# Kernel tuning notes

Measured on AMD Instinct MI355X. Metric: run time of the kernel, lower is better.

The kernel has to match this reference:

```python
import jax, jax.numpy as jnp
import numpy as np

EPS = 1e-6
NEG_SLOPE = 0.2
LN_EPS = 1e-6


def _evn_nonlinearity(x, wa, ba, wb, bb):
    # x: (..., F, D); norm over the vector axis F (axis=-2)
    norm = jnp.linalg.norm(x, axis=-2, keepdims=True)  # (..., 1, D)
    zero_norm = norm <= EPS
    norm = norm + EPS
    h = jax.nn.leaky_relu(norm @ wa + ba, NEG_SLOPE)   # (..., 1, D//2)
    g = h @ wb + bb                                    # (..., 1, D)
    # skip_connection == 0: rescale direction by learned norm gate
    return jnp.where(zero_norm, x, x / norm * g)


def _layernorm(x, scale, bias):
    mean = jnp.mean(x, axis=-1, keepdims=True)
    var = jnp.var(x, axis=-1, keepdims=True)
    return (x - mean) * jax.lax.rsqrt(var + LN_EPS) * scale + bias


def setup_inputs() -> dict:
    key = jax.random.key(0)
    ks = jax.random.split(key, 12)
    B, N, F, D = 8, 2048, 3, 256
    QK, V, H, Q = 512, 512, 8, 64
    dh, dv = QK // H, V // H
    s = lambda *sh: 1.0 / np.sqrt(sh[0])
    return {
        "x": jax.random.normal(ks[0], (B, N, F, D), jnp.float32),
        "lq": jax.random.normal(ks[1], (Q, QK), jnp.float32) * s(QK),
        "w_kv": jax.random.normal(ks[2], (D, QK), jnp.float32) * s(D),
        "w_evn1a": jax.random.normal(ks[3], (QK, QK // 2), jnp.float32) * s(QK),
        "b_evn1a": jnp.zeros((QK // 2,), jnp.float32),
        "w_evn1b": jax.random.normal(ks[4], (QK // 2, QK), jnp.float32) * s(QK // 2),
        "b_evn1b": jnp.zeros((QK,), jnp.float32),
        "wq": jax.random.normal(ks[5], (QK, H, dh), jnp.float32) * s(QK),
        "wk": jax.random.normal(ks[6], (QK, H, dh), jnp.float32) * s(QK),
        "wv": jax.random.normal(ks[7], (QK, H, dv), jnp.float32) * s(QK),
        "ln_q_scale": jnp.ones((dh,), jnp.float32),
        "ln_q_bias": jnp.zeros((dh,), jnp.float32),
        "ln_k_scale": jnp.ones((dh,), jnp.float32),
        "ln_k_bias": jnp.zeros((dh,), jnp.float32),
        "w_out": jax.random.normal(ks[8], (V, V), jnp.float32) * s(V),
        "w_evn2a": jax.random.normal(ks[9], (V, V // 2), jnp.float32) * s(V),
        "b_evn2a": jnp.zeros((V // 2,), jnp.float32),
        "w_evn2b": jax.random.normal(ks[10], (V // 2, V), jnp.float32) * s(V // 2),
        "b_evn2b": jnp.zeros((V,), jnp.float32),
    }


def reference(x, lq, w_kv, w_evn1a, b_evn1a, w_evn1b, b_evn1b, wq, wk, wv,
              ln_q_scale, ln_q_bias, ln_k_scale, ln_k_bias,
              w_out, w_evn2a, b_evn2a, w_evn2b, b_evn2b):
    B, N, F, _ = x.shape
    H = wq.shape[1]
    # EVLinearLeakyReLU: Dense (no bias) + EVN nonlinearity
    kv = _evn_nonlinearity(x @ w_kv, w_evn1a, b_evn1a, w_evn1b, b_evn1b)  # (B,N,F,QK)
    # invariant features: contract vector axis with its channel-mean
    kv_inv = jnp.einsum('bnfd,bnf->bnd', kv, jnp.mean(kv, axis=-1))       # (B,N,QK)
    q = jnp.einsum('qd,dhe->hqe', lq, wq)          # (H,Q,dh)
    k = jnp.einsum('bnd,dhe->hbne', kv_inv, wk)    # (H,B,N,dh)
    v = jnp.einsum('bnfd,dhe->hbnfe', kv, wv)      # (H,B,N,F,dv)
    # normalize_qk
    q = _layernorm(q, ln_q_scale, ln_q_bias)
    k = _layernorm(k, ln_k_scale, ln_k_bias)
    scale = np.sqrt(k.shape[-1]).astype(np.float32)
    attn = jnp.einsum('hqi,hbki->hbqk', q, k)      # (H,B,Q,N)
    attn = jax.nn.softmax(attn / scale, axis=-1)
    resi = jnp.einsum('hbqk,hbkfd->hbqfd', attn, v)  # (H,B,Q,F,dv)
    # 'h b q f d -> b q f (h d)'
    resi = jnp.moveaxis(resi, 0, -2)
    resi = resi.reshape(*resi.shape[:-2], -1)        # (B,Q,F,V)
    resi = _evn_nonlinearity(resi @ w_out, w_evn2a, b_evn2a, w_evn2b, b_evn2b)
    return resi
```

## Files before the change

### kernel.cpp

```cpp
#include <hip/hip_runtime.h>
#include <hip/hip_bf16.h>

typedef _Float16 f16;
typedef __attribute__((ext_vector_type(8))) _Float16 f16x8;
typedef __attribute__((ext_vector_type(4))) _Float16 f16x4;
typedef __attribute__((ext_vector_type(2))) _Float16 f16x2;
typedef __attribute__((ext_vector_type(4))) float floatx4;

constexpr int B  = 8;
constexpr int N  = 2048;
constexpr int Fv = 3;
constexpr int Dd = 256;
constexpr int QK = 512;
constexpr int Vd = 512;
constexpr int Hh = 8;
constexpr int Qq = 64;
constexpr int DH = 64;
constexpr int NT = B * N;
constexpr float EPS = 1e-6f;
constexpr float NEG = 0.2f;
constexpr float LNE = 1e-6f;

#define DEV static __device__ __forceinline__
DEV void split(float v, f16& h, f16& l) { h = (f16)v; l = (f16)(v - (float)h); }

template<int ASRC, int EPI>
__global__ __launch_bounds__(256) void k_gemm3(
    const float* __restrict__ A32,
    const f16* __restrict__ Ah, const f16* __restrict__ Al,
    const f16* __restrict__ Bh, const f16* __restrict__ Bl,
    int Ndim, int Kdim, void* __restrict__ C1, void* __restrict__ C2,
    const float* __restrict__ e0, const float* __restrict__ e1)
{
    __shared__ __align__(16) f16 Ash[128][72];
    __shared__ __align__(16) f16 Asl[128][72];
    __shared__ __align__(16) f16 Bsh[64][72];
    __shared__ __align__(16) f16 Bsl[64][72];

    const int t = threadIdx.x;
    long row0; int col0, boff;
    if (EPI == 5) { row0 = (long)blockIdx.y * 1536 + (long)blockIdx.x * 128; col0 = 0; boff = blockIdx.y * 64; }
    else          { row0 = (long)blockIdx.x * 128; col0 = blockIdx.y * 64; boff = 0; }

    floatx4 acc0[4], acc1[4];
    #pragma unroll
    for (int nt = 0; nt < 4; ++nt)
        #pragma unroll
        for (int j = 0; j < 4; ++j) { acc0[nt][j] = 0.f; acc1[nt][j] = 0.f; }

    const int L = t & 63, w = t >> 6;
    const int kq = (L >> 4) << 3;

    for (int k0 = 0; k0 < Kdim; k0 += 64) {
        if constexpr (ASRC == 1) {
            #pragma unroll
            for (int j = 0; j < 8; ++j) {
                const int i = t + j * 256;
                const int r = i >> 4, c4 = (i & 15) << 2;
                const floatx4 v = *(const floatx4*)&A32[(row0 + r) * Kdim + k0 + c4];
                f16x4 h4, l4;
                #pragma unroll
                for (int m = 0; m < 4; ++m) { h4[m] = (f16)v[m]; l4[m] = (f16)(v[m] - (float)h4[m]); }
                *(f16x4*)&Ash[r][c4] = h4;
                *(f16x4*)&Asl[r][c4] = l4;
            }
        } else {
            #pragma unroll
            for (int j = 0; j < 4; ++j) {
                const int i = t + j * 256;
                const int r = i >> 3, c8 = (i & 7) << 3;
                *(f16x8*)&Ash[r][c8] = *(const f16x8*)&Ah[(row0 + r) * (long)Kdim + k0 + c8];
                *(f16x8*)&Asl[r][c8] = *(const f16x8*)&Al[(row0 + r) * (long)Kdim + k0 + c8];
            }
        }
        #pragma unroll
        for (int j = 0; j < 2; ++j) {
            const int i = t + j * 256;
            const int r = i >> 3, c8 = (i & 7) << 3;
            *(f16x8*)&Bsh[r][c8] = *(const f16x8*)&Bh[(long)(boff + col0 + r) * Kdim + k0 + c8];
            *(f16x8*)&Bsl[r][c8] = *(const f16x8*)&Bl[(long)(boff + col0 + r) * Kdim + k0 + c8];
        }
        __syncthreads();
        #pragma unroll
        for (int kk = 0; kk < 64; kk += 32) {
            const f16x8 ah0 = *(const f16x8*)&Ash[w * 32 + (L & 15)][kk + kq];
            const f16x8 al0 = *(const f16x8*)&Asl[w * 32 + (L & 15)][kk + kq];
            const f16x8 ah1 = *(const f16x8*)&Ash[w * 32 + 16 + (L & 15)][kk + kq];
            const f16x8 al1 = *(const f16x8*)&Asl[w * 32 + 16 + (L & 15)][kk + kq];
            #pragma unroll
            for (int nt = 0; nt < 4; ++nt) {
                const f16x8 bh = *(const f16x8*)&Bsh[nt * 16 + (L & 15)][kk + kq];
                const f16x8 bl = *(const f16x8*)&Bsl[nt * 16 + (L & 15)][kk + kq];
                acc0[nt] = __builtin_amdgcn_mfma_f32_16x16x32_f16(ah0, bh, acc0[nt], 0, 0, 0);
                acc0[nt] = __builtin_amdgcn_mfma_f32_16x16x32_f16(ah0, bl, acc0[nt], 0, 0, 0);
                acc0[nt] = __builtin_amdgcn_mfma_f32_16x16x32_f16(al0, bh, acc0[nt], 0, 0, 0);
                acc1[nt] = __builtin_amdgcn_mfma_f32_16x16x32_f16(ah1, bh, acc1[nt], 0, 0, 0);
                acc1[nt] = __builtin_amdgcn_mfma_f32_16x16x32_f16(ah1, bl, acc1[nt], 0, 0, 0);
                acc1[nt] = __builtin_amdgcn_mfma_f32_16x16x32_f16(al1, bh, acc1[nt], 0, 0, 0);
            }
        }
        __syncthreads();
    }

    const int cb = L & 15;
    #pragma unroll
    for (int rt = 0; rt < 2; ++rt) {
        const floatx4* acc = rt ? acc1 : acc0;
        const int rb = w * 32 + rt * 16 + ((L >> 4) << 2);
        if constexpr (EPI == 0) {
            f16* Ch = (f16*)C1; f16* Cl = (f16*)C2;
            #pragma unroll
            for (int nt = 0; nt < 4; ++nt)
                #pragma unroll
                for (int r = 0; r < 4; ++r) {
                    f16 h, l; split(acc[nt][r], h, l);
                    const long o = (row0 + rb + r) * (long)Ndim + col0 + nt * 16 + cb;
                    Ch[o] = h; Cl[o] = l;
                }
        } else if constexpr (EPI == 1) {
            f16* Ch = (f16*)C1; f16* Cl = (f16*)C2;
            #pragma unroll
            for (int nt = 0; nt < 4; ++nt) {
                const int col = col0 + nt * 16 + cb;
                const float bias = e0[col];
                #pragma unroll
                for (int r = 0; r < 4; ++r) {
                    float v = acc[nt][r] + bias;
                    v = v > 0.f ? v : NEG * v;
                    f16 h, l; split(v, h, l);
                    const long o = (row0 + rb + r) * (long)Ndim + col;
                    Ch[o] = h; Cl[o] = l;
                }
            }
        } else if constexpr (EPI == 2) {
            float* C = (float*)C1;
            #pragma unroll
            for (int nt = 0; nt < 4; ++nt) {
                const int col = col0 + nt * 16 + cb;
                const float bias = e0[col];
                #pragma unroll
                for (int r = 0; r < 4; ++r)
                    C[(row0 + rb + r) * (long)Ndim + col] = acc[nt][r] + bias;
            }
        } else if constexpr (EPI == 3) {
            f16* Ch = (f16*)C1; f16* Cl = (f16*)C2;
            const int h = blockIdx.y;
            #pragma unroll
            for (int r = 0; r < 4; ++r) {
                float s = 0.f, q = 0.f;
                #pragma unroll
                for (int nt = 0; nt < 4; ++nt) { const float v = acc[nt][r]; s += v; q += v * v; }
                s += __shfl_xor(s, 1); q += __shfl_xor(q, 1);
                s += __shfl_xor(s, 2); q += __shfl_xor(q, 2);
                s += __shfl_xor(s, 4); q += __shfl_xor(q, 4);
                s += __shfl_xor(s, 8); q += __shfl_xor(q, 8);
                const float mean = s * (1.f / 64.f);
                const float var  = q * (1.f / 64.f) - mean * mean;
                const float rs   = rsqrtf(var + LNE);
                #pragma unroll
                for (int nt = 0; nt < 4; ++nt) {
                    const int col = nt * 16 + cb;
                    const float v = (acc[nt][r] - mean) * rs * e0[col] + e1[col];
                    f16 hh, ll; split(v, hh, ll);
                    const long o = ((long)h * NT + row0 + rb + r) * 64 + col;
                    Ch[o] = hh; Cl[o] = ll;
                }
            }
        } else {
            float* C = (float*)C1;
            #pragma unroll
            for (int nt = 0; nt < 4; ++nt)
                #pragma unroll
                for (int r = 0; r < 4; ++r) {
                    const long rr = row0 + rb + r - (long)blockIdx.y * 1536;
                    C[rr * 512 + boff + nt * 16 + cb] = acc[nt][r];
                }
        }
    }
}

__global__ __launch_bounds__(512, 4) void k_kv2(
    const float* __restrict__ x,
    const f16* __restrict__ Bh, const f16* __restrict__ Bl,
    f16* __restrict__ Ch, f16* __restrict__ Cl)
{
    __shared__ __align__(16) f16 Ash[2][128][32];
    __shared__ __align__(16) f16 Asl[2][128][32];
    __shared__ __align__(16) f16 Bsh[2][128][32];
    __shared__ __align__(16) f16 Bsl[2][128][32];

    const int t = threadIdx.x;
    const int bx = blockIdx.x;
    const long row0 = (long)(bx >> 2) * 128;
    const int col0 = (bx & 3) * 128;

    const int sr = t >> 2;
    const int sg = t & 3;
    const int spg = ((sg ^ ((sr >> 1) & 3)) << 3);
    const float* ap  = x  + (row0 + sr) * 256 + sg * 8;
    const f16*   bph = Bh + (long)(col0 + sr) * 256 + sg * 8;
    const f16*   bpl = Bl + (long)(col0 + sr) * 256 + sg * 8;

    floatx4 acc[2][4];
    #pragma unroll
    for (int rg = 0; rg < 2; ++rg)
        #pragma unroll
        for (int nt = 0; nt < 4; ++nt)
            #pragma unroll
            for (int j = 0; j < 4; ++j) acc[rg][nt][j] = 0.f;

    const int L = t & 63, w = t >> 6;
    const int wr = (w >> 1) << 5;
    const int wc = (w & 1) << 6;
    const int kqs = (((L >> 4) ^ ((L >> 1) & 3)) << 3);

    floatx4 pa0, pa1; f16x8 pbh, pbl;
    floatx4 qa0, qa1; f16x8 qbh, qbl;

    auto LOADA = [&](int k0) {
        pa0 = *(const floatx4*)&ap[k0];
        pa1 = *(const floatx4*)&ap[k0 + 4];
        pbh = *(const f16x8*)&bph[k0];
        pbl = *(const f16x8*)&bpl[k0];
    };
    auto LOADB = [&](int k0) {
        qa0 = *(const floatx4*)&ap[k0];
        qa1 = *(const floatx4*)&ap[k0 + 4];
        qbh = *(const f16x8*)&bph[k0];
        qbl = *(const f16x8*)&bpl[k0];
    };
    auto WRITEA = [&](int buf) {
        f16x8 h8, l8;
        #pragma unroll
        for (int m = 0; m < 4; ++m) {
            f16 hh, ll;
            split(pa0[m], hh, ll); h8[m] = hh;     l8[m] = ll;
            split(pa1[m], hh, ll); h8[m + 4] = hh; l8[m + 4] = ll;
        }
        *(f16x8*)&Ash[buf][sr][spg] = h8;
        *(f16x8*)&Asl[buf][sr][spg] = l8;
        *(f16x8*)&Bsh[buf][sr][spg] = pbh;
        *(f16x8*)&Bsl[buf][sr][spg] = pbl;
    };
    auto WRITEB = [&](int buf) {
        f16x8 h8, l8;
        #pragma unroll
        for (int m = 0; m < 4; ++m) {
            f16 hh, ll;
            split(qa0[m], hh, ll); h8[m] = hh;     l8[m] = ll;
            split(qa1[m], hh, ll); h8[m + 4] = hh; l8[m + 4] = ll;
        }
        *(f16x8*)&Ash[buf][sr][spg] = h8;
        *(f16x8*)&Asl[buf][sr][spg] = l8;
        *(f16x8*)&Bsh[buf][sr][spg] = qbh;
        *(f16x8*)&Bsl[buf][sr][spg] = qbl;
    };
    auto COMPUTE = [&](int buf) {
        const f16x8 ah0 = *(const f16x8*)&Ash[buf][wr + (L & 15)][kqs];
        const f16x8 al0 = *(const f16x8*)&Asl[buf][wr + (L & 15)][kqs];
        const f16x8 ah1 = *(const f16x8*)&Ash[buf][wr + 16 + (L & 15)][kqs];
        const f16x8 al1 = *(const f16x8*)&Asl[buf][wr + 16 + (L & 15)][kqs];
        #pragma unroll
        for (int nt = 0; nt < 4; ++nt) {
            const f16x8 bh = *(const f16x8*)&Bsh[buf][wc + nt * 16 + (L & 15)][kqs];
            const f16x8 bl = *(const f16x8*)&Bsl[buf][wc + nt * 16 + (L & 15)][kqs];
            acc[0][nt] = __builtin_amdgcn_mfma_f32_16x16x32_f16(ah0, bh, acc[0][nt], 0, 0, 0);
            acc[0][nt] = __builtin_amdgcn_mfma_f32_16x16x32_f16(ah0, bl, acc[0][nt], 0, 0, 0);
            acc[0][nt] = __builtin_amdgcn_mfma_f32_16x16x32_f16(al0, bh, acc[0][nt], 0, 0, 0);
            acc[1][nt] = __builtin_amdgcn_mfma_f32_16x16x32_f16(ah1, bh, acc[1][nt], 0, 0, 0);
            acc[1][nt] = __builtin_amdgcn_mfma_f32_16x16x32_f16(ah1, bl, acc[1][nt], 0, 0, 0);
            acc[1][nt] = __builtin_amdgcn_mfma_f32_16x16x32_f16(al1, bh, acc[1][nt], 0, 0, 0);
        }
    };

    LOADA(0);
    WRITEA(0);
    LOADA(32);
    __syncthreads();

    for (int tt = 0; tt < 8; tt += 2) {
        if (tt + 2 < 8) LOADB((tt + 2) * 32);
        COMPUTE(0);
        if (tt + 1 < 8) WRITEA(1);
        __syncthreads();
        if (tt + 3 < 8) LOADA((tt + 3) * 32);
        COMPUTE(1);
        if (tt + 2 < 8) WRITEB(0);
        __syncthreads();
    }

    const int cb = L & 15;
    #pragma unroll
    for (int rg = 0; rg < 2; ++rg) {
        const int rb = wr + rg * 16 + ((L >> 4) << 2);
        #pragma unroll
        for (int nt = 0; nt < 4; ++nt)
            #pragma unroll
            for (int r = 0; r < 4; ++r) {
                f16 h, l; split(acc[rg][nt][r], h, l);
                const long o = (row0 + rb + r) * 512 + col0 + wc + nt * 16 + cb;
                Ch[o] = h; Cl[o] = l;
            }
    }
}

__global__ __launch_bounds__(256) void k_attn_mfma(
    const f16* __restrict__ qh, const f16* __restrict__ ql,
    const f16* __restrict__ kh, const f16* __restrict__ kl,
    f16* __restrict__ ath, f16* __restrict__ atl, float* __restrict__ lsum_part)
{
    __shared__ __align__(16) f16 Qh[64][72], Ql[64][72];
    __shared__ __align__(16) f16 Kh[64][72], Kl[64][72];

    const int t = threadIdx.x;
    const int bx = blockIdx.x;
    const int hb = bx & 63;
    const int part = bx >> 6;
    const int h = hb >> 3;
    const int L = t & 63, w = t >> 6;
    const int kq = (L >> 4) << 3;

    #pragma unroll
    for (int j = 0; j < 2; ++j) {
        const int i = t + j * 256;
        const int r = i >> 3, c8 = (i & 7) << 3;
        *(f16x8*)&Qh[r][c8] = *(const f16x8*)&qh[((long)h * 64 + r) * 64 + c8];
        *(f16x8*)&Ql[r][c8] = *(const f16x8*)&ql[((long)h * 64 + r) * 64 + c8];
    }
    __syncthreads();

    f16x8 qah[2], qal[2];
    #pragma unroll
    for (int kc = 0; kc < 2; ++kc) {
        qah[kc] = *(const f16x8*)&Qh[w * 16 + (L & 15)][kc * 32 + kq];
        qal[kc] = *(const f16x8*)&Ql[w * 16 + (L & 15)][kc * 32 + kq];
    }

    float psum[4] = {0.f, 0.f, 0.f, 0.f};
    const int rowb = w * 16 + ((L >> 4) << 2);

    for (int nt0 = 0; nt0 < 4; ++nt0) {
        const int n0 = part * 256 + nt0 * 64;
        __syncthreads();
        #pragma unroll
        for (int j = 0; j < 2; ++j) {
            const int i = t + j * 256;
            const int r = i >> 3, c8 = (i & 7) << 3;
            *(f16x8*)&Kh[r][c8] = *(const f16x8*)&kh[((long)hb * N + n0 + r) * 64 + c8];
            *(f16x8*)&Kl[r][c8] = *(const f16x8*)&kl[((long)hb * N + n0 + r) * 64 + c8];
        }
        __syncthreads();

        floatx4 acc[4];
        #pragma unroll
        for (int nt = 0; nt < 4; ++nt)
            #pragma unroll
            for (int j = 0; j < 4; ++j) acc[nt][j] = 0.f;

        #pragma unroll
        for (int kc = 0; kc < 2; ++kc) {
            #pragma unroll
            for (int nt = 0; nt < 4; ++nt) {
                const f16x8 bh = *(const f16x8*)&Kh[nt * 16 + (L & 15)][kc * 32 + kq];
                const f16x8 bl = *(const f16x8*)&Kl[nt * 16 + (L & 15)][kc * 32 + kq];
                acc[nt] = __builtin_amdgcn_mfma_f32_16x16x32_f16(qah[kc], bh, acc[nt], 0, 0, 0);
                acc[nt] = __builtin_amdgcn_mfma_f32_16x16x32_f16(qah[kc], bl, acc[nt], 0, 0, 0);
                acc[nt] = __builtin_amdgcn_mfma_f32_16x16x32_f16(qal[kc], bh, acc[nt], 0, 0, 0);
            }
        }

        #pragma unroll
        for (int nt = 0; nt < 4; ++nt)
            #pragma unroll
            for (int r = 0; r < 4; ++r) {
                const float p = __expf(acc[nt][r] * 0.125f);
                psum[r] += p;
                f16 hh, ll; split(p, hh, ll);
                const long o = ((long)hb * 64 + rowb + r) * N + n0 + nt * 16 + (L & 15);
                ath[o] = hh; atl[o] = ll;
            }
    }

    #pragma unroll
    for (int r = 0; r < 4; ++r) {
        float s = psum[r];
        s += __shfl_xor(s, 1);
        s += __shfl_xor(s, 2);
        s += __shfl_xor(s, 4);
        s += __shfl_xor(s, 8);
        if ((L & 15) == 0) lsum_part[part * 4096 + hb * 64 + rowb + r] = s;
    }
}

__global__ void k_lsum_reduce(const float* __restrict__ part, float* __restrict__ lsum)
{
    const int i = blockIdx.x * 256 + threadIdx.x;
    float s = 0.f;
    #pragma unroll
    for (int p = 0; p < 8; ++p) s += part[p * 4096 + i];
    lsum[i] = s;
}

__global__ __launch_bounds__(512, 4) void k_gemm3T(
    const f16* __restrict__ Ah, const f16* __restrict__ Al,
    const f16* __restrict__ Bh, const f16* __restrict__ Bl,
    const float* __restrict__ lsum,
    f16* __restrict__ Uh, f16* __restrict__ Ul)
{
    __shared__ __align__(16) f16 Ash[2][128][32];
    __shared__ __align__(16) f16 Asl[2][128][32];
    __shared__ __align__(16) f16 Bsh[2][96][32];
    __shared__ __align__(16) f16 Bsl[2][96][32];

    const int t = threadIdx.x;
    const int by = blockIdx.x;
    const int b = by & 7;
    const int rest = by >> 3;
    const int ct = rest & 15;
    const int hp = rest >> 4;
    const int hb0 = b + 16 * hp;
    const int hb1 = hb0 + 8;

    const int ar = t >> 2;
    const int apg = (((t & 3) ^ ((t >> 3) & 3)) << 3);
    const f16* Arh = (ar < 64)
        ? Ah + ((long)hb0 * 64 + ar) * 2048
        : Ah + ((long)hb1 * 64 + (ar - 64)) * 2048;
    const f16* Arl = (ar < 64)
        ? Al + ((long)hb0 * 64 + ar) * 2048
        : Al + ((long)hb1 * 64 + (ar - 64)) * 2048;
    const int aseg = (t & 3) << 3;

    const f16* Bbh = Bh + (long)b * 2048 * 1536 + ct * 96;
    const f16* Bbl = Bl + (long)b * 2048 * 1536 + ct * 96;
    const bool bstage = t < 192;
    const int k2 = t & 15;
    const int cg = t >> 4;

    floatx4 acc[2][3];
    #pragma unroll
    for (int i = 0; i < 2; ++i)
        #pragma unroll
        for (int nt = 0; nt < 3; ++nt)
            #pragma unroll
            for (int j = 0; j < 4; ++j) acc[i][nt][j] = 0.f;

    const int L = t & 63, w = t >> 6;
    const int wr = (w >> 1) << 5;
    const int wc = (w & 1) * 48;
    const int kqs = (((L >> 4) ^ ((L >> 1) & 3)) << 3);

    f16x8 pAh, pAl, pB0h, pB1h, pB0l, pB1l;
    f16x8 qAh, qAl, qB0h, qB1h, qB0l, qB1l;

    auto LOADA = [&](int k0) {
        pAh = *(const f16x8*)&Arh[k0 + aseg];
        pAl = *(const f16x8*)&Arl[k0 + aseg];
        if (bstage) {
            const long r0 = (long)(k0 + 2 * k2) * 1536 + cg * 8;
            pB0h = *(const f16x8*)&Bbh[r0];
            pB1h = *(const f16x8*)&Bbh[r0 + 1536];
            pB0l = *(const f16x8*)&Bbl[r0];
            pB1l = *(const f16x8*)&Bbl[r0 + 1536];
        }
    };
    auto LOADB = [&](int k0) {
        qAh = *(const f16x8*)&Arh[k0 + aseg];
        qAl = *(const f16x8*)&Arl[k0 + aseg];
        if (bstage) {
            const long r0 = (long)(k0 + 2 * k2) * 1536 + cg * 8;
            qB0h = *(const f16x8*)&Bbh[r0];
            qB1h = *(const f16x8*)&Bbh[r0 + 1536];
            qB0l = *(const f16x8*)&Bbl[r0];
            qB1l = *(const f16x8*)&Bbl[r0 + 1536];
        }
    };
    auto WRITEA = [&](int buf) {
        *(f16x8*)&Ash[buf][ar][apg] = pAh;
        *(f16x8*)&Asl[buf][ar][apg] = pAl;
        if (bstage) {
            #pragma unroll
            for (int j = 0; j < 8; ++j) {
                const int hw = ((((k2 >> 2) ^ ((j >> 1) & 3)) << 3) | ((k2 & 3) << 1));
                f16x2 ph; ph[0] = pB0h[j]; ph[1] = pB1h[j];
                f16x2 pl; pl[0] = pB0l[j]; pl[1] = pB1l[j];
                *(f16x2*)&Bsh[buf][cg * 8 + j][hw] = ph;
                *(f16x2*)&Bsl[buf][cg * 8 + j][hw] = pl;
            }
        }
    };
    auto WRITEB = [&](int buf) {
        *(f16x8*)&Ash[buf][ar][apg] = qAh;
        *(f16x8*)&Asl[buf][ar][apg] = qAl;
        if (bstage) {
            #pragma unroll
            for (int j = 0; j < 8; ++j) {
                const int hw = ((((k2 >> 2) ^ ((j >> 1) & 3)) << 3) | ((k2 & 3) << 1));
                f16x2 ph; ph[0] = qB0h[j]; ph[1] = qB1h[j];
                f16x2 pl; pl[0] = qB0l[j]; pl[1] = qB1l[j];
                *(f16x2*)&Bsh[buf][cg * 8 + j][hw] = ph;
                *(f16x2*)&Bsl[buf][cg * 8 + j][hw] = pl;
            }
        }
    };
    auto COMPUTE = [&](int buf) {
        const f16x8 ah0 = *(const f16x8*)&Ash[buf][wr + (L & 15)][kqs];
        const f16x8 al0 = *(const f16x8*)&Asl[buf][wr + (L & 15)][kqs];
        const f16x8 ah1 = *(const f16x8*)&Ash[buf][wr + 16 + (L & 15)][kqs];
        const f16x8 al1 = *(const f16x8*)&Asl[buf][wr + 16 + (L & 15)][kqs];
        #pragma unroll
        for (int nt = 0; nt < 3; ++nt) {
            const f16x8 bh = *(const f16x8*)&Bsh[buf][wc + nt * 16 + (L & 15)][kqs];
            const f16x8 bl = *(const f16x8*)&Bsl[buf][wc + nt * 16 + (L & 15)][kqs];
            acc[0][nt] = __builtin_amdgcn_mfma_f32_16x16x32_f16(ah0, bh, acc[0][nt], 0, 0, 0);
            acc[0][nt] = __builtin_amdgcn_mfma_f32_16x16x32_f16(ah0, bl, acc[0][nt], 0, 0, 0);
            acc[0][nt] = __builtin_amdgcn_mfma_f32_16x16x32_f16(al0, bh, acc[0][nt], 0, 0, 0);
            acc[1][nt] = __builtin_amdgcn_mfma_f32_16x16x32_f16(ah1, bh, acc[1][nt], 0, 0, 0);
            acc[1][nt] = __builtin_amdgcn_mfma_f32_16x16x32_f16(ah1, bl, acc[1][nt], 0, 0, 0);
            acc[1][nt] = __builtin_amdgcn_mfma_f32_16x16x32_f16(al1, bh, acc[1][nt], 0, 0, 0);
        }
    };

    LOADA(0);
    WRITEA(0);
    LOADA(32);
    __syncthreads();

    for (int tt = 0; tt < 64; tt += 2) {
        if (tt + 2 < 64) LOADB((tt + 2) * 32);
        COMPUTE(0);
        if (tt + 1 < 64) WRITEA(1);
        __syncthreads();
        if (tt + 3 < 64) LOADA((tt + 3) * 32);
        COMPUTE(1);
        if (tt + 2 < 64) WRITEB(0);
        __syncthreads();
    }

    const int cb = L & 15;
    #pragma unroll
    for (int rt = 0; rt < 2; ++rt) {
        const int rloc = wr + rt * 16 + ((L >> 4) << 2);
        const int hb = (rloc < 64) ? hb0 : hb1;
        #pragma unroll
        for (int r = 0; r < 4; ++r) {
            const int q = (rloc + r) & 63;
            const float inv = 1.f / lsum[hb * 64 + q];
            #pragma unroll
            for (int nt = 0; nt < 3; ++nt) {
                f16 h, l; split(acc[rt][nt][r] * inv, h, l);
                const long o = ((long)hb * 64 + q) * 1536 + ct * 96 + wc + nt * 16 + cb;
                Uh[o] = h; Ul[o] = l;
            }
        }
    }
}

__global__ void k_castTpair(const float* __restrict__ s, f16* __restrict__ dh,
                            f16* __restrict__ dl, int K, int Nn)
{
    const long i = (long)blockIdx.x * 256 + threadIdx.x;
    if (i >= (long)K * Nn) return;
    const int k = (int)(i / Nn), n = (int)(i - (long)k * Nn);
    f16 h, l; split(s[i], h, l);
    dh[(long)n * K + k] = h;
    dl[(long)n * K + k] = l;
}

__global__ void k_norm(const f16* __restrict__ kh, const f16* __restrict__ kl,
                       f16* __restrict__ nh, f16* __restrict__ nl)
{
    const long i = (long)blockIdx.x * 256 + threadIdx.x;
    const int tk = (int)(i >> 9), c = (int)(i & 511);
    const long base = (long)tk * 1536 + c;
    const float a = (float)kh[base]        + (float)kl[base];
    const float b = (float)kh[base + 512]  + (float)kl[base + 512];
    const float cc = (float)kh[base + 1024] + (float)kl[base + 1024];
    f16 h, l; split(sqrtf(a * a + b * b + cc * cc) + EPS, h, l);
    nh[i] = h; nl[i] = l;
}

__global__ __launch_bounds__(256) void k_gate(
    f16* __restrict__ kh, f16* __restrict__ kl, const float* __restrict__ g,
    f16* __restrict__ kih, f16* __restrict__ kil)
{
    __shared__ float red[3][4];
    const int t = threadIdx.x;
    const int tk = blockIdx.x;
    float kv[2][3];
    float ps0 = 0.f, ps1 = 0.f, ps2 = 0.f;
    #pragma unroll
    for (int j = 0; j < 2; ++j) {
        const int c = t + j * 256;
        const long base = (long)tk * 1536 + c;
        const float k0 = (float)kh[base]        + (float)kl[base];
        const float k1 = (float)kh[base + 512]  + (float)kl[base + 512];
        const float k2 = (float)kh[base + 1024] + (float)kl[base + 1024];
        const float nr = sqrtf(k0 * k0 + k1 * k1 + k2 * k2);
        const float gv = g[(long)tk * 512 + c];
        const float s = (nr <= EPS) ? 1.f : gv / (nr + EPS);
        kv[j][0] = k0 * s; kv[j][1] = k1 * s; kv[j][2] = k2 * s;
        f16 h, l;
        split(kv[j][0], h, l); kh[base] = h;        kl[base] = l;
        split(kv[j][1], h, l); kh[base + 512] = h;  kl[base + 512] = l;
        split(kv[j][2], h, l); kh[base + 1024] = h; kl[base + 1024] = l;
        ps0 += kv[j][0]; ps1 += kv[j][1]; ps2 += kv[j][2];
    }
    for (int off = 32; off; off >>= 1) {
        ps0 += __shfl_down(ps0, off);
        ps1 += __shfl_down(ps1, off);
        ps2 += __shfl_down(ps2, off);
    }
    if ((t & 63) == 0) { red[0][t >> 6] = ps0; red[1][t >> 6] = ps1; red[2][t >> 6] = ps2; }
    __syncthreads();
    const float m0 = (red[0][0] + red[0][1] + red[0][2] + red[0][3]) * (1.f / 512.f);
    const float m1 = (red[1][0] + red[1][1] + red[1][2] + red[1][3]) * (1.f / 512.f);
    const float m2 = (red[2][0] + red[2][1] + red[2][2] + red[2][3]) * (1.f / 512.f);
    #pragma unroll
    for (int j = 0; j < 2; ++j) {
        const int c = t + j * 256;
        f16 h, l; split(kv[j][0] * m0 + kv[j][1] * m1 + kv[j][2] * m2, h, l);
        kih[(long)tk * 512 + c] = h;
        kil[(long)tk * 512 + c] = l;
    }
}

__global__ __launch_bounds__(256) void k_gate2(
    const f16* __restrict__ rph, const f16* __restrict__ rpl,
    const float* __restrict__ g2, float* __restrict__ out)
{
    const int t = threadIdx.x;
    const int tk = blockIdx.x;
    #pragma unroll
    for (int j = 0; j < 2; ++j) {
        const int c = t + j * 256;
        const long base = (long)tk * 1536 + c;
        const float r0 = (float)rph[base]        + (float)rpl[base];
        const float r1 = (float)rph[base + 512]  + (float)rpl[base + 512];
        const float r2 = (float)rph[base + 1024] + (float)rpl[base + 1024];
        const float nr = sqrtf(r0 * r0 + r1 * r1 + r2 * r2);
        const float gv = g2[(long)tk * 512 + c];
        const float s = (nr <= EPS) ? 1.f : gv / (nr + EPS);
        out[base]        = r0 * s;
        out[base + 512]  = r1 * s;
        out[base + 1024] = r2 * s;
    }
}

__global__ __launch_bounds__(256) void k_qproj(
    const float* __restrict__ lq, const float* __restrict__ wq,
    const float* __restrict__ lns, const float* __restrict__ lnb,
    f16* __restrict__ qh, f16* __restrict__ ql)
{
    __shared__ float cs[QK];
    const int t = threadIdx.x;
    const int qi = blockIdx.x;
    const float* cp = lq + (long)qi * QK;
    for (int i = t; i < QK; i += 256) cs[i] = cp[i];
    __syncthreads();

    float a0 = 0, a1 = 0;
    #pragma unroll 4
    for (int d = 0; d < QK; ++d) {
        const float c = cs[d];
        a0 += c * wq[d * QK + t];
        a1 += c * wq[d * QK + t + 256];
    }
    float s0 = a0, q0 = a0 * a0, s1 = a1, q1 = a1 * a1;
    for (int off = 32; off; off >>= 1) {
        s0 += __shfl_down(s0, off); q0 += __shfl_down(q0, off);
        s1 += __shfl_down(s1, off); q1 += __shfl_down(q1, off);
    }
    s0 = __shfl(s0, 0); q0 = __shfl(q0, 0);
    s1 = __shfl(s1, 0); q1 = __shfl(q1, 0);
    const float mean0 = s0 * (1.f / 64.f), var0 = q0 * (1.f / 64.f) - mean0 * mean0;
    const float mean1 = s1 * (1.f / 64.f), var1 = q1 * (1.f / 64.f) - mean1 * mean1;
    const int e = t & 63;
    const float sc = lns[e], bi = lnb[e];
    const float r0 = (a0 - mean0) * rsqrtf(var0 + LNE) * sc + bi;
    const float r1 = (a1 - mean1) * rsqrtf(var1 + LNE) * sc + bi;
    const int h0 = t >> 6, h1 = h0 + 4;
    f16 h, l;
    split(r0, h, l);
    qh[((long)h0 * Qq + qi) * DH + e] = h;
    ql[((long)h0 * Qq + qi) * DH + e] = l;
    split(r1, h, l);
    qh[((long)h1 * Qq + qi) * DH + e] = h;
    ql[((long)h1 * Qq + qi) * DH + e] = l;
}

extern "C" void kernel_launch(void* const* d_in, const int* in_sizes, int n_in,
                              void* d_out, int out_size, void* d_ws, size_t ws_size,
                              hipStream_t stream)
{
    const float* x    = (const float*)d_in[0];
    const float* lq   = (const float*)d_in[1];
    const float* w_kv = (const float*)d_in[2];
    const float* w1a  = (const float*)d_in[3];
    const float* b1a  = (const float*)d_in[4];
    const float* w1b  = (const float*)d_in[5];
    const float* b1b  = (const float*)d_in[6];
    const float* wq   = (const float*)d_in[7];
    const float* wk   = (const float*)d_in[8];
    const float* wv   = (const float*)d_in[9];
    const float* lqs  = (const float*)d_in[10];
    const float* lqb  = (const float*)d_in[11];
    const float* lks  = (const float*)d_in[12];
    const float* lkb  = (const float*)d_in[13];
    const float* wo   = (const float*)d_in[14];
    const float* w2a  = (const float*)d_in[15];
    const float* b2a  = (const float*)d_in[16];
    const float* w2b  = (const float*)d_in[17];
    const float* b2b  = (const float*)d_in[18];

    char* ws = (char*)d_ws;
    f16* wkvTh = (f16*)(ws + 0);
    f16* wkvTl = (f16*)(ws + 262144);
    f16* w1aTh = (f16*)(ws + 524288);
    f16* w1aTl = (f16*)(ws + 786432);
    f16* w1bTh = (f16*)(ws + 1048576);
    f16* w1bTl = (f16*)(ws + 1310720);
    f16* wkTh  = (f16*)(ws + 1572864);
    f16* wkTl  = (f16*)(ws + 2097152);
    f16* wvTh  = (f16*)(ws + 2621440);
    f16* wvTl  = (f16*)(ws + 3145728);
    f16*   qhp   = (f16*)(ws + 3670016);
    f16*   qlp   = (f16*)(ws + 3735552);
    float* lsum  = (float*)(ws + 3801088);
    f16* woTh  = (f16*)(ws + 3817472);
    f16* woTl  = (f16*)(ws + 4341760);
    f16* w2aTh = (f16*)(ws + 4866048);
    f16* w2aTl = (f16*)(ws + 5128192);
    f16* w2bTh = (f16*)(ws + 5390336);
    f16* w2bTl = (f16*)(ws + 5652480);
    float* lsum_part = (float*)(ws + 5914624);
    f16* nh    = (f16*)(ws + 6946816);
    f16* nl    = (f16*)(ws + 23724032);
    f16* kih   = nh;
    f16* kil   = nl;
    f16* ath   = (f16*)(ws + 6946816);
    f16* atl   = (f16*)(ws + 23724032);
    f16*   rph  = (f16*)(ws + 6946816);
    f16*   rpl  = (f16*)(ws + 8519680);
    f16*   n2h  = (f16*)(ws + 10092544);
    f16*   n2l  = (f16*)(ws + 10616832);
    f16*   h2h  = (f16*)(ws + 11141120);
    f16*   h2l  = (f16*)(ws + 11403264);
    float* g2   = (float*)(ws + 11665408);
    f16* hbh   = (f16*)(ws + 40501248);
    f16* hbl   = (f16*)(ws + 48889856);
    float* resiT = (float*)(ws + 40501248);
    f16* kvh   = (f16*)(ws + 57278464);
    f16* kvl   = (f16*)(ws + 107610112);
    float* g    = (float*)(ws + 157941760);
    f16* khb   = (f16*)(ws + 157941760);
    f16* klb   = (f16*)(ws + 174718976);
    f16* Uh    = (f16*)(ws + 157941760);
    f16* Ul    = (f16*)(ws + 170524672);
    float* out  = (float*)d_out;

    k_castTpair<<<512,  256, 0, stream>>>(w_kv, wkvTh, wkvTl, Dd, QK);
    k_castTpair<<<512,  256, 0, stream>>>(w1a,  w1aTh, w1aTl, QK, 256);
    k_castTpair<<<512,  256, 0, stream>>>(w1b,  w1bTh, w1bTl, 256, QK);
    k_castTpair<<<1024, 256, 0, stream>>>(wk,   wkTh,  wkTl,  QK, QK);
    k_castTpair<<<1024, 256, 0, stream>>>(wv,   wvTh,  wvTl,  QK, QK);
    k_castTpair<<<1024, 256, 0, stream>>>(wo,   woTh,  woTl,  Vd, Vd);
    k_castTpair<<<512,  256, 0, stream>>>(w2a,  w2aTh, w2aTl, Vd, 256);
    k_castTpair<<<512,  256, 0, stream>>>(w2b,  w2bTh, w2bTl, 256, Vd);

    k_kv2<<<1536, 512, 0, stream>>>(x, wkvTh, wkvTl, kvh, kvl);
    k_norm<<<32768, 256, 0, stream>>>(kvh, kvl, nh, nl);
    k_gemm3<0, 1><<<dim3(128, 4), 256, 0, stream>>>(
        nullptr, nh, nl, w1aTh, w1aTl, 256, QK, hbh, hbl, b1a, nullptr);
    k_gemm3<0, 2><<<dim3(128, 8), 256, 0, stream>>>(
        nullptr, hbh, hbl, w1bTh, w1bTl, QK, 256, g, nullptr, b1b, nullptr);
    k_gate<<<NT, 256, 0, stream>>>(kvh, kvl, g, kih, kil);
    k_gemm3<0, 3><<<dim3(128, 8), 256, 0, stream>>>(
        nullptr, kih, kil, wkTh, wkTl, QK, QK, khb, klb, lks, lkb);
    k_qproj<<<Qq, 256, 0, stream>>>(lq, wq, lqs, lqb, qhp, qlp);
    k_attn_mfma<<<512, 256, 0, stream>>>(qhp, qlp, khb, klb, ath, atl, lsum_part);
    k_lsum_reduce<<<16, 256, 0, stream>>>(lsum_part, lsum);
    k_gemm3T<<<512, 512, 0, stream>>>(ath, atl, kvh, kvl, lsum, Uh, Ul);
    k_gemm3<0, 5><<<dim3(12, 8), 256, 0, stream>>>(
        nullptr, Uh, Ul, wvTh, wvTl, 64, QK, resiT, nullptr, nullptr, nullptr);
    k_gemm3<1, 0><<<dim3(12, 8), 256, 0, stream>>>(
        resiT, nullptr, nullptr, woTh, woTl, Vd, Vd, rph, rpl, nullptr, nullptr);
    k_norm<<<1024, 256, 0, stream>>>(rph, rpl, n2h, n2l);
    k_gemm3<0, 1><<<dim3(4, 4), 256, 0, stream>>>(
        nullptr, n2h, n2l, w2aTh, w2aTl, 256, Vd, h2h, h2l, b2a, nullptr);
    k_gemm3<0, 2><<<dim3(4, 8), 256, 0, stream>>>(
        nullptr, h2h, h2l, w2bTh, w2bTl, Vd, 256, g2, nullptr, b2b, nullptr);
    k_gate2<<<B * Qq, 256, 0, stream>>>(rph, rpl, g2, out);
}
```

Before: 561.7 us.

## Replace split-fp16 GEMMs for EVN1 and K projection with pipelined 128x128 tile kernel

Adds a k_pgemm kernel that uses the double-buffered, register-prefetched 128x128 tile scheme from k_kv2, with swizzled LDS layouts and 512 threads. It replaces the k_gemm3 calls for the two EVN1 MLP layers and the LayerNorm K projection, keeping their bias/leaky-relu, bias, and LayerNorm epilogues. The larger tiles are meant to raise operand reuse and hide global-load latency behind MFMA work. In exchange, each block uses more registers and LDS, and there are fewer blocks for the smaller GEMMs.

```diff
diff --git a/kernel.cpp b/kernel.cpp
--- a/kernel.cpp
+++ b/kernel.cpp
@@ -142,14 +142,283 @@
                 for (int r = 0; r < 4; ++r)
                     C[(row0 + rb + r) * (long)Ndim + col] = acc[nt][r] + bias;
             }
-        } else if constexpr (EPI == 3) {
+        } else {
+            float* C = (float*)C1;
+            #pragma unroll
+            for (int nt = 0; nt < 4; ++nt)
+                #pragma unroll
+                for (int r = 0; r < 4; ++r) {
+                    const long rr = row0 + rb + r - (long)blockIdx.y * 1536;
+                    C[rr * 512 + boff + nt * 16 + cb] = acc[nt][r];
+                }
+        }
+    }
+}
+
+__global__ __launch_bounds__(512, 4) void k_kv2(
+    const float* __restrict__ x,
+    const f16* __restrict__ Bh, const f16* __restrict__ Bl,
+    f16* __restrict__ Ch, f16* __restrict__ Cl)
+{
+    __shared__ __align__(16) f16 Ash[2][128][32];
+    __shared__ __align__(16) f16 Asl[2][128][32];
+    __shared__ __align__(16) f16 Bsh[2][128][32];
+    __shared__ __align__(16) f16 Bsl[2][128][32];
+
+    const int t = threadIdx.x;
+    const int bx = blockIdx.x;
+    const long row0 = (long)(bx >> 2) * 128;
+    const int col0 = (bx & 3) * 128;
+
+    const int sr = t >> 2;
+    const int sg = t & 3;
+    const int spg = ((sg ^ ((sr >> 1) & 3)) << 3);
+    const float* ap  = x  + (row0 + sr) * 256 + sg * 8;
+    const f16*   bph = Bh + (long)(col0 + sr) * 256 + sg * 8;
+    const f16*   bpl = Bl + (long)(col0 + sr) * 256 + sg * 8;
+
+    floatx4 acc[2][4];
+    #pragma unroll
+    for (int rg = 0; rg < 2; ++rg)
+        #pragma unroll
+        for (int nt = 0; nt < 4; ++nt)
+            #pragma unroll
+            for (int j = 0; j < 4; ++j) acc[rg][nt][j] = 0.f;
+
+    const int L = t & 63, w = t >> 6;
+    const int wr = (w >> 1) << 5;
+    const int wc = (w & 1) << 6;
+    const int kqs = (((L >> 4) ^ ((L >> 1) & 3)) << 3);
+
+    floatx4 pa0, pa1; f16x8 pbh, pbl;
+    floatx4 qa0, qa1; f16x8 qbh, qbl;
+
+    auto LOADA = [&](int k0) {
+        pa0 = *(const floatx4*)&ap[k0];
+        pa1 = *(const floatx4*)&ap[k0 + 4];
+        pbh = *(const f16x8*)&bph[k0];
+        pbl = *(const f16x8*)&bpl[k0];
+    };
+    auto LOADB = [&](int k0) {
+        qa0 = *(const floatx4*)&ap[k0];
+        qa1 = *(const floatx4*)&ap[k0 + 4];
+        qbh = *(const f16x8*)&bph[k0];
+        qbl = *(const f16x8*)&bpl[k0];
+    };
+    auto WRITEA = [&](int buf) {
+        f16x8 h8, l8;
+        #pragma unroll
+        for (int m = 0; m < 4; ++m) {
+            f16 hh, ll;
+            split(pa0[m], hh, ll); h8[m] = hh;     l8[m] = ll;
+            split(pa1[m], hh, ll); h8[m + 4] = hh; l8[m + 4] = ll;
+        }
+        *(f16x8*)&Ash[buf][sr][spg] = h8;
+        *(f16x8*)&Asl[buf][sr][spg] = l8;
+        *(f16x8*)&Bsh[buf][sr][spg] = pbh;
+        *(f16x8*)&Bsl[buf][sr][spg] = pbl;
+    };
+    auto WRITEB = [&](int buf) {
+        f16x8 h8, l8;
+        #pragma unroll
+        for (int m = 0; m < 4; ++m) {
+            f16 hh, ll;
+            split(qa0[m], hh, ll); h8[m] = hh;     l8[m] = ll;
+            split(qa1[m], hh, ll); h8[m + 4] = hh; l8[m + 4] = ll;
+        }
+        *(f16x8*)&Ash[buf][sr][spg] = h8;
+        *(f16x8*)&Asl[buf][sr][spg] = l8;
+        *(f16x8*)&Bsh[buf][sr][spg] = qbh;
+        *(f16x8*)&Bsl[buf][sr][spg] = qbl;
+    };
+    auto COMPUTE = [&](int buf) {
+        const f16x8 ah0 = *(const f16x8*)&Ash[buf][wr + (L & 15)][kqs];
+        const f16x8 al0 = *(const f16x8*)&Asl[buf][wr + (L & 15)][kqs];
+        const f16x8 ah1 = *(const f16x8*)&Ash[buf][wr + 16 + (L & 15)][kqs];
+        const f16x8 al1 = *(const f16x8*)&Asl[buf][wr + 16 + (L & 15)][kqs];
+        #pragma unroll
+        for (int nt = 0; nt < 4; ++nt) {
+            const f16x8 bh = *(const f16x8*)&Bsh[buf][wc + nt * 16 + (L & 15)][kqs];
+            const f16x8 bl = *(const f16x8*)&Bsl[buf][wc + nt * 16 + (L & 15)][kqs];
+            acc[0][nt] = __builtin_amdgcn_mfma_f32_16x16x32_f16(ah0, bh, acc[0][nt], 0, 0, 0);
+            acc[0][nt] = __builtin_amdgcn_mfma_f32_16x16x32_f16(ah0, bl, acc[0][nt], 0, 0, 0);
+            acc[0][nt] = __builtin_amdgcn_mfma_f32_16x16x32_f16(al0, bh, acc[0][nt], 0, 0, 0);
+            acc[1][nt] = __builtin_amdgcn_mfma_f32_16x16x32_f16(ah1, bh, acc[1][nt], 0, 0, 0);
+            acc[1][nt] = __builtin_amdgcn_mfma_f32_16x16x32_f16(ah1, bl, acc[1][nt], 0, 0, 0);
+            acc[1][nt] = __builtin_amdgcn_mfma_f32_16x16x32_f16(al1, bh, acc[1][nt], 0, 0, 0);
+        }
+    };
+
+    LOADA(0);
+    WRITEA(0);
+    LOADA(32);
+    __syncthreads();
+
+    for (int tt = 0; tt < 8; tt += 2) {
+        if (tt + 2 < 8) LOADB((tt + 2) * 32);
+        COMPUTE(0);
+        if (tt + 1 < 8) WRITEA(1);
+        __syncthreads();
+        if (tt + 3 < 8) LOADA((tt + 3) * 32);
+        COMPUTE(1);
+        if (tt + 2 < 8) WRITEB(0);
+        __syncthreads();
+    }
+
+    const int cb = L & 15;
+    #pragma unroll
+    for (int rg = 0; rg < 2; ++rg) {
+        const int rb = wr + rg * 16 + ((L >> 4) << 2);
+        #pragma unroll
+        for (int nt = 0; nt < 4; ++nt)
+            #pragma unroll
+            for (int r = 0; r < 4; ++r) {
+                f16 h, l; split(acc[rg][nt][r], h, l);
+                const long o = (row0 + rb + r) * 512 + col0 + wc + nt * 16 + cb;
+                Ch[o] = h; Cl[o] = l;
+            }
+    }
+}
+
+template<int EPI>
+__global__ __launch_bounds__(512, 4) void k_pgemm(
+    const f16* __restrict__ Ah, const f16* __restrict__ Al,
+    const f16* __restrict__ Bh, const f16* __restrict__ Bl,
+    int Ndim, int Kdim, int ncs,
+    void* __restrict__ C1, void* __restrict__ C2,
+    const float* __restrict__ e0, const float* __restrict__ e1)
+{
+    __shared__ __align__(16) f16 Ash[2][128][32];
+    __shared__ __align__(16) f16 Asl[2][128][32];
+    __shared__ __align__(16) f16 Bsh[2][128][32];
+    __shared__ __align__(16) f16 Bsl[2][128][32];
+
+    const int t = threadIdx.x;
+    const int bx = blockIdx.x;
+    const int col0 = (bx & ((1 << ncs) - 1)) << 7;
+    const long row0 = (long)(bx >> ncs) * 128;
+
+    const int sr = t >> 2;
+    const int sg = t & 3;
+    const int spg = ((sg ^ ((sr >> 1) & 3)) << 3);
+    const f16* aph = Ah + (row0 + sr) * (long)Kdim + sg * 8;
+    const f16* apl = Al + (row0 + sr) * (long)Kdim + sg * 8;
+    const f16* bph = Bh + (long)(col0 + sr) * Kdim + sg * 8;
+    const f16* bpl = Bl + (long)(col0 + sr) * Kdim + sg * 8;
+
+    floatx4 acc[2][4];
+    #pragma unroll
+    for (int rg = 0; rg < 2; ++rg)
+        #pragma unroll
+        for (int nt = 0; nt < 4; ++nt)
+            #pragma unroll
+            for (int j = 0; j < 4; ++j) acc[rg][nt][j] = 0.f;
+
+    const int L = t & 63, w = t >> 6;
+    const int wr = (w >> 1) << 5;
+    const int wc = (w & 1) << 6;
+    const int kqs = (((L >> 4) ^ ((L >> 1) & 3)) << 3);
+
+    f16x8 pah, pal, pbh, pbl;
+    f16x8 qah, qal, qbh, qbl;
+
+    auto LOADA = [&](int k0) {
+        pah = *(const f16x8*)&aph[k0];
+        pal = *(const f16x8*)&apl[k0];
+        pbh = *(const f16x8*)&bph[k0];
+        pbl = *(const f16x8*)&bpl[k0];
+    };
+    auto LOADB = [&](int k0) {
+        qah = *(const f16x8*)&aph[k0];
+        qal = *(const f16x8*)&apl[k0];
+        qbh = *(const f16x8*)&bph[k0];
+        qbl = *(const f16x8*)&bpl[k0];
+    };
+    auto WRITEA = [&](int buf) {
+        *(f16x8*)&Ash[buf][sr][spg] = pah;
+        *(f16x8*)&Asl[buf][sr][spg] = pal;
+        *(f16x8*)&Bsh[buf][sr][spg] = pbh;
+        *(f16x8*)&Bsl[buf][sr][spg] = pbl;
+    };
+    auto WRITEB = [&](int buf) {
+        *(f16x8*)&Ash[buf][sr][spg] = qah;
+        *(f16x8*)&Asl[buf][sr][spg] = qal;
+        *(f16x8*)&Bsh[buf][sr][spg] = qbh;
+        *(f16x8*)&Bsl[buf][sr][spg] = qbl;
+    };
+    auto COMPUTE = [&](int buf) {
+        const f16x8 ah0 = *(const f16x8*)&Ash[buf][wr + (L & 15)][kqs];
+        const f16x8 al0 = *(const f16x8*)&Asl[buf][wr + (L & 15)][kqs];
+        const f16x8 ah1 = *(const f16x8*)&Ash[buf][wr + 16 + (L & 15)][kqs];
+        const f16x8 al1 = *(const f16x8*)&Asl[buf][wr + 16 + (L & 15)][kqs];
+        #pragma unroll
+        for (int nt = 0; nt < 4; ++nt) {
+            const f16x8 bh = *(const f16x8*)&Bsh[buf][wc + nt * 16 + (L & 15)][kqs];
+            const f16x8 bl = *(const f16x8*)&Bsl[buf][wc + nt * 16 + (L & 15)][kqs];
+            acc[0][nt] = __builtin_amdgcn_mfma_f32_16x16x32_f16(ah0, bh, acc[0][nt], 0, 0, 0);
+            acc[0][nt] = __builtin_amdgcn_mfma_f32_16x16x32_f16(ah0, bl, acc[0][nt], 0, 0, 0);
+            acc[0][nt] = __builtin_amdgcn_mfma_f32_16x16x32_f16(al0, bh, acc[0][nt], 0, 0, 0);
+            acc[1][nt] = __builtin_amdgcn_mfma_f32_16x16x32_f16(ah1, bh, acc[1][nt], 0, 0, 0);
+            acc[1][nt] = __builtin_amdgcn_mfma_f32_16x16x32_f16(ah1, bl, acc[1][nt], 0, 0, 0);
+            acc[1][nt] = __builtin_amdgcn_mfma_f32_16x16x32_f16(al1, bh, acc[1][nt], 0, 0, 0);
+        }
+    };
+
+    const int ntiles = Kdim >> 5;
+
+    LOADA(0);
+    WRITEA(0);
+    LOADA(32);
+    __syncthreads();
+
+    for (int tt = 0; tt < ntiles; tt += 2) {
+        if (tt + 2 < ntiles) LOADB((tt + 2) * 32);
+        COMPUTE(0);
+        if (tt + 1 < ntiles) WRITEA(1);
+        __syncthreads();
+        if (tt + 3 < ntiles) LOADA((tt + 3) * 32);
+        COMPUTE(1);
+        if (tt + 2 < ntiles) WRITEB(0);
+        __syncthreads();
+    }
+
+    const int cb = L & 15;
+    #pragma unroll
+    for (int rg = 0; rg < 2; ++rg) {
+        const int rb = wr + rg * 16 + ((L >> 4) << 2);
+        if constexpr (EPI == 1) {
             f16* Ch = (f16*)C1; f16* Cl = (f16*)C2;
-            const int h = blockIdx.y;
+            #pragma unroll
+            for (int nt = 0; nt < 4; ++nt) {
+                const int col = col0 + wc + nt * 16 + cb;
+                const float bias = e0[col];
+                #pragma unroll
+                for (int r = 0; r < 4; ++r) {
+                    float v = acc[rg][nt][r] + bias;
+                    v = v > 0.f ? v : NEG * v;
+                    f16 h, l; split(v, h, l);
+                    const long o = (row0 + rb + r) * (long)Ndim + col;
+                    Ch[o] = h; Cl[o] = l;
+                }
+            }
+        } else if constexpr (EPI == 2) {
+            float* C = (float*)C1;
+            #pragma unroll
+            for (int nt = 0; nt < 4; ++nt) {
+                const int col = col0 + wc + nt * 16 + cb;
+                const float bias = e0[col];
+                #pragma unroll
+                for (int r = 0; r < 4; ++r)
+                    C[(row0 + rb + r) * (long)Ndim + col] = acc[rg][nt][r] + bias;
+            }
+        } else {
+            f16* Ch = (f16*)C1; f16* Cl = (f16*)C2;
+            const int h = (col0 + wc) >> 6;
             #pragma unroll
             for (int r = 0; r < 4; ++r) {
                 float s = 0.f, q = 0.f;
                 #pragma unroll
-                for (int nt = 0; nt < 4; ++nt) { const float v = acc[nt][r]; s += v; q += v * v; }
+                for (int nt = 0; nt < 4; ++nt) { const float v = acc[rg][nt][r]; s += v; q += v * v; }
                 s += __shfl_xor(s, 1); q += __shfl_xor(q, 1);
                 s += __shfl_xor(s, 2); q += __shfl_xor(q, 2);
                 s += __shfl_xor(s, 4); q += __shfl_xor(q, 4);
@@ -159,148 +428,14 @@
                 const float rs   = rsqrtf(var + LNE);
                 #pragma unroll
                 for (int nt = 0; nt < 4; ++nt) {
-                    const int col = nt * 16 + cb;
-                    const float v = (acc[nt][r] - mean) * rs * e0[col] + e1[col];
+                    const int colh = nt * 16 + cb;
+                    const float v = (acc[rg][nt][r] - mean) * rs * e0[colh] + e1[colh];
                     f16 hh, ll; split(v, hh, ll);
-                    const long o = ((long)h * NT + row0 + rb + r) * 64 + col;
+                    const long o = ((long)h * NT + row0 + rb + r) * 64 + colh;
                     Ch[o] = hh; Cl[o] = ll;
                 }
             }
-        } else {
-            float* C = (float*)C1;
-            #pragma unroll
-            for (int nt = 0; nt < 4; ++nt)
-                #pragma unroll
-                for (int r = 0; r < 4; ++r) {
-                    const long rr = row0 + rb + r - (long)blockIdx.y * 1536;
-                    C[rr * 512 + boff + nt * 16 + cb] = acc[nt][r];
-                }
-        }
-    }
-}
-
-__global__ __launch_bounds__(512, 4) void k_kv2(
-    const float* __restrict__ x,
-    const f16* __restrict__ Bh, const f16* __restrict__ Bl,
-    f16* __restrict__ Ch, f16* __restrict__ Cl)
-{
-    __shared__ __align__(16) f16 Ash[2][128][32];
-    __shared__ __align__(16) f16 Asl[2][128][32];
-    __shared__ __align__(16) f16 Bsh[2][128][32];
-    __shared__ __align__(16) f16 Bsl[2][128][32];
-
-    const int t = threadIdx.x;
-    const int bx = blockIdx.x;
-    const long row0 = (long)(bx >> 2) * 128;
-    const int col0 = (bx & 3) * 128;
-
-    const int sr = t >> 2;
-    const int sg = t & 3;
-    const int spg = ((sg ^ ((sr >> 1) & 3)) << 3);
-    const float* ap  = x  + (row0 + sr) * 256 + sg * 8;
-    const f16*   bph = Bh + (long)(col0 + sr) * 256 + sg * 8;
-    const f16*   bpl = Bl + (long)(col0 + sr) * 256 + sg * 8;
-
-    floatx4 acc[2][4];
-    #pragma unroll
-    for (int rg = 0; rg < 2; ++rg)
-        #pragma unroll
-        for (int nt = 0; nt < 4; ++nt)
-            #pragma unroll
-            for (int j = 0; j < 4; ++j) acc[rg][nt][j] = 0.f;
-
-    const int L = t & 63, w = t >> 6;
-    const int wr = (w >> 1) << 5;
-    const int wc = (w & 1) << 6;
-    const int kqs = (((L >> 4) ^ ((L >> 1) & 3)) << 3);
-
-    floatx4 pa0, pa1; f16x8 pbh, pbl;
-    floatx4 qa0, qa1; f16x8 qbh, qbl;
-
-    auto LOADA = [&](int k0) {
-        pa0 = *(const floatx4*)&ap[k0];
-        pa1 = *(const floatx4*)&ap[k0 + 4];
-        pbh = *(const f16x8*)&bph[k0];
-        pbl = *(const f16x8*)&bpl[k0];
-    };
-    auto LOADB = [&](int k0) {
-        qa0 = *(const floatx4*)&ap[k0];
-        qa1 = *(const floatx4*)&ap[k0 + 4];
-        qbh = *(const f16x8*)&bph[k0];
-        qbl = *(const f16x8*)&bpl[k0];
-    };
-    auto WRITEA = [&](int buf) {
-        f16x8 h8, l8;
-        #pragma unroll
-        for (int m = 0; m < 4; ++m) {
-            f16 hh, ll;
-            split(pa0[m], hh, ll); h8[m] = hh;     l8[m] = ll;
-            split(pa1[m], hh, ll); h8[m + 4] = hh; l8[m + 4] = ll;
-        }
-        *(f16x8*)&Ash[buf][sr][spg] = h8;
-        *(f16x8*)&Asl[buf][sr][spg] = l8;
-        *(f16x8*)&Bsh[buf][sr][spg] = pbh;
-        *(f16x8*)&Bsl[buf][sr][spg] = pbl;
-    };
-    auto WRITEB = [&](int buf) {
-        f16x8 h8, l8;
-        #pragma unroll
-        for (int m = 0; m < 4; ++m) {
-            f16 hh, ll;
-            split(qa0[m], hh, ll); h8[m] = hh;     l8[m] = ll;
-            split(qa1[m], hh, ll); h8[m + 4] = hh; l8[m + 4] = ll;
-        }
-        *(f16x8*)&Ash[buf][sr][spg] = h8;
-        *(f16x8*)&Asl[buf][sr][spg] = l8;
-        *(f16x8*)&Bsh[buf][sr][spg] = qbh;
-        *(f16x8*)&Bsl[buf][sr][spg] = qbl;
-    };
-    auto COMPUTE = [&](int buf) {
-        const f16x8 ah0 = *(const f16x8*)&Ash[buf][wr + (L & 15)][kqs];
-        const f16x8 al0 = *(const f16x8*)&Asl[buf][wr + (L & 15)][kqs];
-        const f16x8 ah1 = *(const f16x8*)&Ash[buf][wr + 16 + (L & 15)][kqs];
-        const f16x8 al1 = *(const f16x8*)&Asl[buf][wr + 16 + (L & 15)][kqs];
-        #pragma unroll
-        for (int nt = 0; nt < 4; ++nt) {
-            const f16x8 bh = *(const f16x8*)&Bsh[buf][wc + nt * 16 + (L & 15)][kqs];
-            const f16x8 bl = *(const f16x8*)&Bsl[buf][wc + nt * 16 + (L & 15)][kqs];
-            acc[0][nt] = __builtin_amdgcn_mfma_f32_16x16x32_f16(ah0, bh, acc[0][nt], 0, 0, 0);
-            acc[0][nt] = __builtin_amdgcn_mfma_f32_16x16x32_f16(ah0, bl, acc[0][nt], 0, 0, 0);
-            acc[0][nt] = __builtin_amdgcn_mfma_f32_16x16x32_f16(al0, bh, acc[0][nt], 0, 0, 0);
-            acc[1][nt] = __builtin_amdgcn_mfma_f32_16x16x32_f16(ah1, bh, acc[1][nt], 0, 0, 0);
-            acc[1][nt] = __builtin_amdgcn_mfma_f32_16x16x32_f16(ah1, bl, acc[1][nt], 0, 0, 0);
-            acc[1][nt] = __builtin_amdgcn_mfma_f32_16x16x32_f16(al1, bh, acc[1][nt], 0, 0, 0);
-        }
-    };
-
-    LOADA(0);
-    WRITEA(0);
-    LOADA(32);
-    __syncthreads();
-
-    for (int tt = 0; tt < 8; tt += 2) {
-        if (tt + 2 < 8) LOADB((tt + 2) * 32);
-        COMPUTE(0);
-        if (tt + 1 < 8) WRITEA(1);
-        __syncthreads();
-        if (tt + 3 < 8) LOADA((tt + 3) * 32);
-        COMPUTE(1);
-        if (tt + 2 < 8) WRITEB(0);
-        __syncthreads();
-    }
-
-    const int cb = L & 15;
-    #pragma unroll
-    for (int rg = 0; rg < 2; ++rg) {
-        const int rb = wr + rg * 16 + ((L >> 4) << 2);
-        #pragma unroll
-        for (int nt = 0; nt < 4; ++nt)
-            #pragma unroll
-            for (int r = 0; r < 4; ++r) {
-                f16 h, l; split(acc[rg][nt][r], h, l);
-                const long o = (row0 + rb + r) * 512 + col0 + wc + nt * 16 + cb;
-                Ch[o] = h; Cl[o] = l;
-            }
+        }
     }
 }
 
@@ -770,13 +905,13 @@
 
     k_kv2<<<1536, 512, 0, stream>>>(x, wkvTh, wkvTl, kvh, kvl);
     k_norm<<<32768, 256, 0, stream>>>(kvh, kvl, nh, nl);
-    k_gemm3<0, 1><<<dim3(128, 4), 256, 0, stream>>>(
-        nullptr, nh, nl, w1aTh, w1aTl, 256, QK, hbh, hbl, b1a, nullptr);
-    k_gemm3<0, 2><<<dim3(128, 8), 256, 0, stream>>>(
-        nullptr, hbh, hbl, w1bTh, w1bTl, QK, 256, g, nullptr, b1b, nullptr);
+    k_pgemm<1><<<256, 512, 0, stream>>>(
+        nh, nl, w1aTh, w1aTl, 256, 512, 1, hbh, hbl, b1a, nullptr);
+    k_pgemm<2><<<512, 512, 0, stream>>>(
+        hbh, hbl, w1bTh, w1bTl, 512, 256, 2, g, nullptr, b1b, nullptr);
     k_gate<<<NT, 256, 0, stream>>>(kvh, kvl, g, kih, kil);
-    k_gemm3<0, 3><<<dim3(128, 8), 256, 0, stream>>>(
-        nullptr, kih, kil, wkTh, wkTl, QK, QK, khb, klb, lks, lkb);
+    k_pgemm<3><<<512, 512, 0, stream>>>(
+        kih, kil, wkTh, wkTl, 512, 512, 2, khb, klb, lks, lkb);
     k_qproj<<<Qq, 256, 0, stream>>>(lq, wq, lqs, lqb, qhp, qlp);
     k_attn_mfma<<<512, 256, 0, stream>>>(qhp, qlp, khb, klb, ath, atl, lsum_part);
     k_lsum_reduce<<<16, 256, 0, stream>>>(lsum_part, lsum);
```

After: 571.8 us. No clear change (+1.8%).
